# Kernel optimization log

Hardware: AMD Instinct MI355X
Metric: run time of the kernel (lower is better)

The kernel has to match this reference:

```python
import jax, jax.numpy as jnp
import numpy as np

EPS = 1e-5
DN = ('NCHW', 'OIHW', 'NCHW')

def _conv(x, w, b):
    y = jax.lax.conv_general_dilated(x, w, (1, 1), 'SAME', dimension_numbers=DN)
    return y + b.reshape(1, -1, 1, 1)

def _bn(x, g, bt, m, v):
    # inference-mode BatchNorm2d
    scale = g * jax.lax.rsqrt(v + EPS)
    return (x - m.reshape(1, -1, 1, 1)) * scale.reshape(1, -1, 1, 1) + bt.reshape(1, -1, 1, 1)


def setup_inputs() -> dict:
    key = jax.random.key(0)
    ks = jax.random.split(key, 12)
    B, C, H, W = 32, 1, 1024, 1024
    inp = {
        'x':  jax.random.normal(ks[0], (B, C, H, W), jnp.float32),
        # conv3x3_bn_r (shared module, used 3 times)
        'wa': jax.random.normal(ks[1], (1, 1, 3, 3), jnp.float32) * 0.2,
        'ba': jnp.zeros((1,), jnp.float32),
        'ga': jnp.ones((1,), jnp.float32),
        'bta': jnp.zeros((1,), jnp.float32),
        'ma': jax.random.normal(ks[2], (1,), jnp.float32) * 0.1,
        'va': jax.random.uniform(ks[3], (1,), jnp.float32) + 0.5,
        # conv3x3_bn
        'wb': jax.random.normal(ks[4], (1, 1, 3, 3), jnp.float32) * 0.2,
        'bb': jnp.zeros((1,), jnp.float32),
        'gb': jnp.ones((1,), jnp.float32),
        'btb': jnp.zeros((1,), jnp.float32),
        'mb': jax.random.normal(ks[5], (1,), jnp.float32) * 0.1,
        'vb': jax.random.uniform(ks[6], (1,), jnp.float32) + 0.5,
        # conv1x1_bn
        'wc': jax.random.normal(ks[7], (1, 1, 1, 1), jnp.float32) * 0.2,
        'bc': jnp.zeros((1,), jnp.float32),
        'gc': jnp.ones((1,), jnp.float32),
        'btc': jnp.zeros((1,), jnp.float32),
        'mc': jax.random.normal(ks[8], (1,), jnp.float32) * 0.1,
        'vc': jax.random.uniform(ks[9], (1,), jnp.float32) + 0.5,
        # conv3x3_r
        'wd': jax.random.normal(ks[10], (1, 1, 3, 3), jnp.float32) * 0.2,
        'bd': jnp.zeros((1,), jnp.float32),
        # conv1x1
        'we': jax.random.normal(ks[11], (1, 1, 1, 1), jnp.float32) * 0.2,
        'be': jnp.zeros((1,), jnp.float32),
    }
    return inp


def reference(x, wa, ba, ga, bta, ma, va, wb, bb, gb, btb, mb, vb,
              wc, bc, gc, btc, mc, vc, wd, bd, we, be):
    # t = 0 (top-left corner): right->left cummax + bottom->up cummax
    # conv3x3_bn_r is one shared module; x1 == x2 in the original.
    x1 = jax.nn.relu(_bn(_conv(x, wa, ba), ga, bta, ma, va))
    i1 = jax.lax.cummax(x1, axis=3, reverse=True)  # RightLeftMaxPooling
    i2 = jax.lax.cummax(x1, axis=2, reverse=True)  # DownUpMaxPooling
    b1 = _bn(_conv(i1 + i2, wb, bb), gb, btb, mb, vb)
    b2 = _bn(_conv(x, wc, bc), gc, btc, mc, vc)
    s = jax.nn.relu(b1 + b2)
    out = jax.nn.relu(_bn(_conv(s, wa, ba), ga, bta, ma, va))  # shared conv3x3_bn_r again
    out = jax.nn.relu(_conv(out, wd, bd))
    out = _conv(out, we, be)
    return out
```

## Files before the change

kernel.cpp:

```cpp
#include <hip/hip_runtime.h>
#include <math.h>

#define EPS 1e-5f
constexpr int IMG_H = 1024;
constexpr int IMG_W = 1024;
constexpr int NIMG  = 32;

__device__ __forceinline__ float frelu(float v) { return fmaxf(v, 0.f); }

__global__ __launch_bounds__(256) void k_front(
    const float* __restrict__ x,
    const float* __restrict__ wa, const float* __restrict__ ba,
    const float* __restrict__ ga, const float* __restrict__ bta,
    const float* __restrict__ ma, const float* __restrict__ va,
    float* __restrict__ M8, float* __restrict__ M8part, float* __restrict__ I1S)
{
    const int bid   = blockIdx.x;
    const int img   = bid >> 7;
    const int strip = bid & 127;
    const int lane  = threadIdx.x & 63;
    const int wv    = threadIdx.x >> 6;
    const int rb    = strip * 8 + wv * 2;

    const float scale = ga[0] * rsqrtf(va[0] + EPS);
    float w_s[9];
#pragma unroll
    for (int k = 0; k < 9; ++k) w_s[k] = wa[k] * scale;
    const float bias = (ba[0] - ma[0]) * scale + bta[0];

    const float* xim = x + (size_t)img * IMG_H * IMG_W;

    float4 X[4][4];
#pragma unroll
    for (int ri = 0; ri < 4; ++ri) {
        const int gr = rb - 1 + ri;
        if (gr >= 0 && gr < IMG_H) {
            const float4* rp = (const float4*)(xim + (size_t)gr * IMG_W);
#pragma unroll
            for (int q = 0; q < 4; ++q) X[ri][q] = rp[lane + 64 * q];
        } else {
#pragma unroll
            for (int q = 0; q < 4; ++q) X[ri][q] = make_float4(0.f, 0.f, 0.f, 0.f);
        }
    }

    float4 wm[4], w1r1[4];
#pragma unroll
    for (int rr = 0; rr < 2; ++rr) {
        float4 v[4];
#pragma unroll
        for (int q = 0; q < 4; ++q) {
            float acc0 = bias, acc1 = bias, acc2 = bias, acc3 = bias;
#pragma unroll
            for (int dy = 0; dy < 3; ++dy) {
                float4 C = X[rr + dy][q];
                float Lw = __shfl_up(C.w, 1, 64);
                float Bq = 0.f;
                if (q > 0) Bq = __shfl(X[rr + dy][q - 1].w, 63, 64);
                if (lane == 0) Lw = Bq;
                float Rx = __shfl_down(C.x, 1, 64);
                float Aq = 0.f;
                if (q < 3) Aq = __shfl(X[rr + dy][q + 1].x, 0, 64);
                if (lane == 63) Rx = Aq;
                const float w0 = w_s[3 * dy], w1 = w_s[3 * dy + 1], w2 = w_s[3 * dy + 2];
                acc0 += w0 * Lw  + w1 * C.x + w2 * C.y;
                acc1 += w0 * C.x + w1 * C.y + w2 * C.z;
                acc2 += w0 * C.y + w1 * C.z + w2 * C.w;
                acc3 += w0 * C.z + w1 * C.w + w2 * Rx;
            }
            v[q] = make_float4(frelu(acc0), frelu(acc1), frelu(acc2), frelu(acc3));
        }

        float sW[4], T4[4], e[4];
#pragma unroll
        for (int q = 0; q < 4; ++q) {
            float s3 = v[q].w;
            float s2 = fmaxf(v[q].z, s3);
            float s1 = fmaxf(v[q].y, s2);
            float s0 = fmaxf(v[q].x, s1);
            sW[q] = s3;
            float mm = s0;
#pragma unroll
            for (int off = 1; off < 64; off <<= 1) {
                float o = __shfl_down(mm, off, 64);
                if (lane + off < 64) mm = fmaxf(mm, o);
            }
            T4[q] = __shfl(mm, 0, 64);
            float ex = __shfl_down(mm, 1, 64);
            if (lane == 63) ex = -INFINITY;
            e[q] = ex;
        }
        float Rr[4];
        Rr[3] = -INFINITY;
        Rr[2] = T4[3];
        Rr[1] = fmaxf(T4[2], Rr[2]);
        Rr[0] = fmaxf(T4[1], Rr[1]);

        if ((lane & 7) == 0) {
            const int r = rb + rr;
#pragma unroll
            for (int q = 0; q < 4; ++q) {
                const float val = fmaxf(sW[q], fmaxf(e[q], Rr[q]));
                I1S[((size_t)img * IMG_H + r) * 32 + (q * 8 + (lane >> 3))] = val;
            }
        }

        if (rr == 0) {
#pragma unroll
            for (int q = 0; q < 4; ++q) wm[q] = v[q];
        } else {
#pragma unroll
            for (int q = 0; q < 4; ++q) {
                wm[q].x = fmaxf(wm[q].x, v[q].x); wm[q].y = fmaxf(wm[q].y, v[q].y);
                wm[q].z = fmaxf(wm[q].z, v[q].z); wm[q].w = fmaxf(wm[q].w, v[q].w);
            }
#pragma unroll
            for (int q = 0; q < 4; ++q) w1r1[q] = v[q];
        }
    }

    __shared__ float4 wmax[5][256];
#pragma unroll
    for (int q = 0; q < 4; ++q) wmax[wv][64 * q + lane] = wm[q];
    if (wv == 1) {
#pragma unroll
        for (int q = 0; q < 4; ++q) wmax[4][64 * q + lane] = w1r1[q];
    }
    __syncthreads();

    const int tid = threadIdx.x;
    float4 a0 = wmax[0][tid], a1 = wmax[1][tid], a2 = wmax[2][tid], a3 = wmax[3][tid];
    float4 f;
    f.x = fmaxf(fmaxf(a0.x, a1.x), fmaxf(a2.x, a3.x));
    f.y = fmaxf(fmaxf(a0.y, a1.y), fmaxf(a2.y, a3.y));
    f.z = fmaxf(fmaxf(a0.z, a1.z), fmaxf(a2.z, a3.z));
    f.w = fmaxf(fmaxf(a0.w, a1.w), fmaxf(a2.w, a3.w));
    ((float4*)(M8 + ((size_t)img * 128 + strip) * IMG_W))[tid] = f;

    if (strip >= 8 && (strip & 7) == 0) {
        float4 r3v = wmax[4][tid];
        float4 fp;
        fp.x = fmaxf(r3v.x, fmaxf(a2.x, a3.x));
        fp.y = fmaxf(r3v.y, fmaxf(a2.y, a3.y));
        fp.z = fmaxf(r3v.z, fmaxf(a2.z, a3.z));
        fp.w = fmaxf(r3v.w, fmaxf(a2.w, a3.w));
        ((float4*)(M8part + ((size_t)img * 15 + ((strip >> 3) - 1)) * IMG_W))[tid] = fp;
    }
}

__global__ __launch_bounds__(256) void k_seed2(
    const float* __restrict__ M8, const float* __restrict__ M8part,
    float* __restrict__ I2S)
{
    const int gid = blockIdx.x * 256 + threadIdx.x;
    const int img = gid >> 10;
    const int c   = gid & 1023;
    const float* mp = M8 + (size_t)img * 128 * IMG_W + c;

    float run = 0.f;
#pragma unroll 7
    for (int s = 127; s >= 9; --s) {
        run = fmaxf(run, mp[(size_t)s * IMG_W]);
        if ((s & 7) == 1) {
            const int m = (s - 9) >> 3;
            const size_t o = ((size_t)img * 15 + m) * IMG_W + c;
            I2S[o] = fmaxf(run, M8part[o]);
        }
    }
}

#define PITCH 44
__global__ __launch_bounds__(256, 6) void k_tile(
    const float* __restrict__ x,
    const float* __restrict__ I1S, const float* __restrict__ I2S,
    const float* __restrict__ wa, const float* __restrict__ ba,
    const float* __restrict__ ga, const float* __restrict__ bta,
    const float* __restrict__ ma, const float* __restrict__ va,
    const float* __restrict__ wb, const float* __restrict__ bb,
    const float* __restrict__ gb, const float* __restrict__ btb,
    const float* __restrict__ mb, const float* __restrict__ vb,
    const float* __restrict__ wc, const float* __restrict__ bc,
    const float* __restrict__ gcp, const float* __restrict__ btc,
    const float* __restrict__ mc, const float* __restrict__ vc,
    const float* __restrict__ wd, const float* __restrict__ bd,
    const float* __restrict__ we, const float* __restrict__ be,
    float* __restrict__ out)
{
    __shared__ float B1[70 * PITCH];
    __shared__ float B2[68 * PITCH];
    __shared__ float P[4][PITCH];

    const int bid = blockIdx.x;
    const int img = bid >> 9;
    const int tr  = (bid >> 5) & 15;
    const int tc  = bid & 31;
    const int r0  = tr * 64, c0 = tc * 32;
    const int tid = threadIdx.x;
    const int lane = tid & 63;
    const int wv   = tid >> 6;

    const float* xim = x + (size_t)img * IMG_H * IMG_W;

    float i2sv = 0.f;
    if (tr < 15 && lane < 38) {
        const int col = c0 - 3 + lane;
        if ((unsigned)col < (unsigned)IMG_W)
            i2sv = I2S[((size_t)img * 15 + tr) * IMG_W + col];
    }
    const int g0 = wv * 18;
    const int nrows = (wv == 3) ? 16 : 18;
    float seed1v = 0.f;
    if (lane < nrows && tc < 31) {
        const int row = r0 - 3 + g0 + lane;
        if ((unsigned)row < (unsigned)IMG_H)
            seed1v = I1S[((size_t)img * IMG_H + row) * 32 + (tc + 1)];
    }

    const float sa = ga[0] * rsqrtf(va[0] + EPS);
    float was[9];
#pragma unroll
    for (int k = 0; k < 9; ++k) was[k] = wa[k] * sa;
    const float biasa = (ba[0] - ma[0]) * sa + bta[0];

    const float sb = gb[0] * rsqrtf(vb[0] + EPS);
    float wbs[9];
#pragma unroll
    for (int k = 0; k < 9; ++k) wbs[k] = wb[k] * sb;
    const float biasb = (bb[0] - mb[0]) * sb + btb[0];

    const float sc = gcp[0] * rsqrtf(vc[0] + EPS);
    const float kc = wc[0] * sc;
    const float biasc = (bc[0] - mc[0]) * sc + btc[0];

    float wd9[9];
#pragma unroll
    for (int k = 0; k < 9; ++k) wd9[k] = wd[k];
    const float bd0 = bd[0], we0 = we[0], be0 = be[0];

    if (tid < 180) {
        const int mi = tid / 10, mj = tid - mi * 10;
        const int wr0 = mi * 4, wc0 = mj * 4;
        const int gr0 = r0 - 4 + wr0;
        const int gc0 = c0 - 4 + wc0;
        const bool fastC = (gc0 >= 0) && (gc0 + 5 < IMG_W);
        float w[6][6];
#pragma unroll
        for (int rr = 0; rr < 6; ++rr) {
            const int gr = gr0 + rr;
            if ((unsigned)gr < (unsigned)IMG_H) {
                const float* rp = xim + (size_t)gr * IMG_W;
                if (fastC) {
                    float4 a4 = *(const float4*)(rp + gc0);
                    float2 b2 = *(const float2*)(rp + gc0 + 4);
                    w[rr][0] = a4.x; w[rr][1] = a4.y; w[rr][2] = a4.z;
                    w[rr][3] = a4.w; w[rr][4] = b2.x; w[rr][5] = b2.y;
                } else {
#pragma unroll
                    for (int j = 0; j < 6; ++j) {
                        const int gc = gc0 + j;
                        w[rr][j] = ((unsigned)gc < (unsigned)IMG_W) ? rp[gc] : 0.f;
                    }
                }
            } else {
#pragma unroll
                for (int j = 0; j < 6; ++j) w[rr][j] = 0.f;
            }
        }
#pragma unroll
        for (int rr = 0; rr < 4; ++rr) {
            if (wr0 + rr < 70) {
                const int grx = r0 - 3 + wr0 + rr;
                float res4[4];
#pragma unroll
                for (int cc = 0; cc < 4; ++cc) {
                    float acc = biasa;
#pragma unroll
                    for (int dy = 0; dy < 3; ++dy)
#pragma unroll
                        for (int dx = 0; dx < 3; ++dx)
                            acc += was[3 * dy + dx] * w[rr + dy][cc + dx];
                    const int gcx = c0 - 3 + wc0 + cc;
                    float val = 0.f;
                    if ((unsigned)grx < (unsigned)IMG_H && (unsigned)gcx < (unsigned)IMG_W)
                        val = frelu(acc);
                    res4[cc] = val;
                }
                *(float4*)&B1[(wr0 + rr) * PITCH + wc0] =
                    make_float4(res4[0], res4[1], res4[2], res4[3]);
            }
        }
    }
    __syncthreads();

    {
        float pm = 0.f;
        if (lane < 38) {
            for (int k = 0; k < nrows; ++k)
                pm = fmaxf(pm, B1[(g0 + k) * PITCH + lane]);
            P[wv][lane] = pm;
        }
    }
    __syncthreads();

    {
        float run = i2sv;
#pragma unroll
        for (int w2 = 1; w2 < 4; ++w2)
            if (w2 > wv && lane < 38) run = fmaxf(run, P[w2][lane]);
#pragma unroll 6
        for (int k = 0; k < 18; ++k) {
            if (k < nrows) {
                const int lr = nrows - 1 - k;
                const int wr = g0 + lr;
                const float xv = (lane < 38) ? B1[wr * PITCH + lane] : 0.f;
                float mm = xv;
#pragma unroll
                for (int off = 1; off < 64; off <<= 1) {
                    float o = __shfl_down(mm, off, 64);
                    if (lane + off < 64) mm = fmaxf(mm, o);
                }
                const float sd = __shfl(seed1v, lr, 64);
                const float i1v = fmaxf(mm, sd);
                run = fmaxf(run, xv);
                const int row = r0 - 3 + wr;
                const int col = c0 - 3 + lane;
                const bool inb = ((unsigned)row < (unsigned)IMG_H) &&
                                 ((unsigned)col < (unsigned)IMG_W);
                if (lane < 38)
                    B1[wr * PITCH + lane] = inb ? (i1v + run) : 0.f;
            }
        }
    }
    __syncthreads();

    if (tid < 153) {
        const int mi = tid / 9, mj = tid - mi * 9;
        const int si0 = mi * 4, sj0 = mj * 4;
        float win[6][6];
#pragma unroll
        for (int r = 0; r < 6; ++r) {
            const float* p = &B1[(si0 + r) * PITCH + sj0];
            float4 a4 = *(const float4*)p;
            float2 b2 = *(const float2*)(p + 4);
            win[r][0] = a4.x; win[r][1] = a4.y; win[r][2] = a4.z;
            win[r][3] = a4.w; win[r][4] = b2.x; win[r][5] = b2.y;
        }
#pragma unroll
        for (int a = 0; a < 4; ++a) {
            float res4[4];
#pragma unroll
            for (int b = 0; b < 4; ++b) {
                float acc = biasb;
#pragma unroll
                for (int dy = 0; dy < 3; ++dy)
#pragma unroll
                    for (int dx = 0; dx < 3; ++dx)
                        acc += wbs[3 * dy + dx] * win[a + dy][b + dx];
                const int gr = r0 - 2 + si0 + a, gc = c0 - 2 + sj0 + b;
                float sres = 0.f;
                if ((unsigned)gr < (unsigned)IMG_H && (unsigned)gc < (unsigned)IMG_W) {
                    const float xv = xim[(size_t)gr * IMG_W + gc];
                    sres = frelu(acc + xv * kc + biasc);
                }
                res4[b] = sres;
            }
            *(float4*)&B2[(si0 + a) * PITCH + sj0] =
                make_float4(res4[0], res4[1], res4[2], res4[3]);
        }
    }
    __syncthreads();

    if (tid < 153) {
        const int mi = tid / 9, mj = tid - mi * 9;
        const int ai0 = mi * 4, aj0 = mj * 4;
        float win[6][6];
#pragma unroll
        for (int r = 0; r < 6; ++r) {
            const int rrow = (ai0 + r < 68) ? (ai0 + r) : 67;
            const float* p = &B2[rrow * PITCH + aj0];
            float4 a4 = *(const float4*)p;
            float2 b2 = *(const float2*)(p + 4);
            win[r][0] = a4.x; win[r][1] = a4.y; win[r][2] = a4.z;
            win[r][3] = a4.w; win[r][4] = b2.x; win[r][5] = b2.y;
        }
#pragma unroll
        for (int a = 0; a < 4; ++a) {
            if (ai0 + a < 66) {
                float res4[4];
#pragma unroll
                for (int b = 0; b < 4; ++b) {
                    float acc = biasa;
#pragma unroll
                    for (int dy = 0; dy < 3; ++dy)
#pragma unroll
                        for (int dx = 0; dx < 3; ++dx)
                            acc += was[3 * dy + dx] * win[a + dy][b + dx];
                    const int gr = r0 - 1 + ai0 + a, gc = c0 - 1 + aj0 + b;
                    float r1 = 0.f;
                    if ((unsigned)gr < (unsigned)IMG_H && (unsigned)gc < (unsigned)IMG_W)
                        r1 = frelu(acc);
                    res4[b] = r1;
                }
                *(float4*)&B1[(ai0 + a) * PITCH + aj0] =
                    make_float4(res4[0], res4[1], res4[2], res4[3]);
            }
        }
    }
    __syncthreads();

    {
        const int oi0 = (tid >> 3) * 2, oj0 = (tid & 7) * 4;
        float win[4][6];
#pragma unroll
        for (int r = 0; r < 4; ++r) {
            const float* p = &B1[(oi0 + r) * PITCH + oj0];
            float4 a4 = *(const float4*)p;
            float2 b2 = *(const float2*)(p + 4);
            win[r][0] = a4.x; win[r][1] = a4.y; win[r][2] = a4.z;
            win[r][3] = a4.w; win[r][4] = b2.x; win[r][5] = b2.y;
        }
        float* oim = out + (size_t)img * IMG_H * IMG_W;
#pragma unroll
        for (int a = 0; a < 2; ++a) {
            float res4[4];
#pragma unroll
            for (int b = 0; b < 4; ++b) {
                float acc = bd0;
#pragma unroll
                for (int dy = 0; dy < 3; ++dy)
#pragma unroll
                    for (int dx = 0; dx < 3; ++dx)
                        acc += wd9[3 * dy + dx] * win[a + dy][b + dx];
                res4[b] = frelu(acc) * we0 + be0;
            }
            *(float4*)&oim[(size_t)(r0 + oi0 + a) * IMG_W + (c0 + oj0)] =
                make_float4(res4[0], res4[1], res4[2], res4[3]);
        }
    }
}

extern "C" void kernel_launch(void* const* d_in, const int* in_sizes, int n_in,
                              void* d_out, int out_size, void* d_ws, size_t ws_size,
                              hipStream_t stream)
{
    const float* x   = (const float*)d_in[0];
    const float* wa  = (const float*)d_in[1];
    const float* ba  = (const float*)d_in[2];
    const float* ga  = (const float*)d_in[3];
    const float* bta = (const float*)d_in[4];
    const float* ma  = (const float*)d_in[5];
    const float* va  = (const float*)d_in[6];
    const float* wb  = (const float*)d_in[7];
    const float* bb  = (const float*)d_in[8];
    const float* gb  = (const float*)d_in[9];
    const float* btb = (const float*)d_in[10];
    const float* mb  = (const float*)d_in[11];
    const float* vb  = (const float*)d_in[12];
    const float* wc  = (const float*)d_in[13];
    const float* bc  = (const float*)d_in[14];
    const float* gcp = (const float*)d_in[15];
    const float* btc = (const float*)d_in[16];
    const float* mc  = (const float*)d_in[17];
    const float* vc  = (const float*)d_in[18];
    const float* wd  = (const float*)d_in[19];
    const float* bd  = (const float*)d_in[20];
    const float* we  = (const float*)d_in[21];
    const float* be  = (const float*)d_in[22];

    float* outp   = (float*)d_out;
    float* M8     = (float*)d_ws;
    float* M8part = M8 + (size_t)NIMG * 128 * IMG_W;
    float* I1S    = M8part + (size_t)NIMG * 15 * IMG_W;
    float* I2S    = I1S + (size_t)NIMG * IMG_H * 32;

    k_front<<<dim3(NIMG * 128), dim3(256), 0, stream>>>(
        x, wa, ba, ga, bta, ma, va, M8, M8part, I1S);
    k_seed2<<<dim3(128), dim3(256), 0, stream>>>(M8, M8part, I2S);
    k_tile<<<dim3(NIMG * 16 * 32), dim3(256), 0, stream>>>(
        x, I1S, I2S, wa, ba, ga, bta, ma, va, wb, bb, gb, btb, mb, vb,
        wc, bc, gcp, btc, mc, vc, wd, bd, we, be, outp);
}
```

Baseline: 511.9 us.

## Stage input tile in shared memory and reuse it for the 1x1 branch

Loads the 72x40 input halo tile into a new shared buffer BA with coalesced float4 loads, replacing the per-thread overlapping global 6x6 window loads. The conv1x1 branch then reads x from this shared tile into registers instead of issuing scalar global loads. After that, BA is reused as the storage that B2 used to have, which keeps total LDS about the same. Interior tiles skip the per-pixel image-boundary checks. The cost is an extra barrier and a 16-float register array that could add register pressure at 6 blocks per CU.

```diff
diff --git a/kernel.cpp b/kernel.cpp
--- a/kernel.cpp
+++ b/kernel.cpp
@@ -186,9 +186,9 @@
     const float* __restrict__ we, const float* __restrict__ be,
     float* __restrict__ out)
 {
+    __shared__ float BA[72 * PITCH];
     __shared__ float B1[70 * PITCH];
-    __shared__ float B2[68 * PITCH];
-    __shared__ float P[4][PITCH];
+    __shared__ float Pm[4][PITCH];
 
     const int bid = blockIdx.x;
     const int img = bid >> 9;
@@ -198,6 +198,7 @@
     const int tid = threadIdx.x;
     const int lane = tid & 63;
     const int wv   = tid >> 6;
+    const bool intr = (tr >= 1) && (tr <= 14) && (tc >= 1) && (tc <= 30);
 
     const float* xim = x + (size_t)img * IMG_H * IMG_W;
 
@@ -237,39 +238,59 @@
     for (int k = 0; k < 9; ++k) wd9[k] = wd[k];
     const float bd0 = bd[0], we0 = we[0], be0 = be[0];
 
+    if (intr) {
+        const float* xs = xim + (size_t)(r0 - 4) * IMG_W + (c0 - 4);
+#pragma unroll
+        for (int it = 0; it < 3; ++it) {
+            const int f = tid + it * 256;
+            if (f < 720) {
+                const int row = f / 10, cg = f - row * 10;
+                float4 v = *(const float4*)(xs + (size_t)row * IMG_W + 4 * cg);
+                *(float4*)&BA[row * PITCH + 4 * cg] = v;
+            }
+        }
+    } else {
+#pragma unroll
+        for (int it = 0; it < 3; ++it) {
+            const int f = tid + it * 256;
+            if (f < 720) {
+                const int row = f / 10, cg = f - row * 10;
+                const int gr = r0 - 4 + row;
+                const int gc = c0 - 4 + 4 * cg;
+                float4 v = make_float4(0.f, 0.f, 0.f, 0.f);
+                if ((unsigned)gr < (unsigned)IMG_H) {
+                    const float* rp = xim + (size_t)gr * IMG_W;
+                    if (gc >= 0 && gc + 3 < IMG_W) {
+                        v = *(const float4*)(rp + gc);
+                    } else {
+                        if ((unsigned)(gc)     < (unsigned)IMG_W) v.x = rp[gc];
+                        if ((unsigned)(gc + 1) < (unsigned)IMG_W) v.y = rp[gc + 1];
+                        if ((unsigned)(gc + 2) < (unsigned)IMG_W) v.z = rp[gc + 2];
+                        if ((unsigned)(gc + 3) < (unsigned)IMG_W) v.w = rp[gc + 3];
+                    }
+                }
+                *(float4*)&BA[row * PITCH + 4 * cg] = v;
+            }
+        }
+    }
+    __syncthreads();
+
     if (tid < 180) {
         const int mi = tid / 10, mj = tid - mi * 10;
         const int wr0 = mi * 4, wc0 = mj * 4;
-        const int gr0 = r0 - 4 + wr0;
-        const int gc0 = c0 - 4 + wc0;
-        const bool fastC = (gc0 >= 0) && (gc0 + 5 < IMG_W);
         float w[6][6];
 #pragma unroll
-        for (int rr = 0; rr < 6; ++rr) {
-            const int gr = gr0 + rr;
-            if ((unsigned)gr < (unsigned)IMG_H) {
-                const float* rp = xim + (size_t)gr * IMG_W;
-                if (fastC) {
-                    float4 a4 = *(const float4*)(rp + gc0);
-                    float2 b2 = *(const float2*)(rp + gc0 + 4);
-                    w[rr][0] = a4.x; w[rr][1] = a4.y; w[rr][2] = a4.z;
-                    w[rr][3] = a4.w; w[rr][4] = b2.x; w[rr][5] = b2.y;
-                } else {
-#pragma unroll
-                    for (int j = 0; j < 6; ++j) {
-                        const int gc = gc0 + j;
-                        w[rr][j] = ((unsigned)gc < (unsigned)IMG_W) ? rp[gc] : 0.f;
-                    }
-                }
-            } else {
-#pragma unroll
-                for (int j = 0; j < 6; ++j) w[rr][j] = 0.f;
-            }
+        for (int r = 0; r < 6; ++r) {
+            const int br = (wr0 + r < 72) ? (wr0 + r) : 71;
+            const float* p = &BA[br * PITCH + wc0];
+            float4 a4 = *(const float4*)p;
+            float2 b2 = *(const float2*)(p + 4);
+            w[r][0] = a4.x; w[r][1] = a4.y; w[r][2] = a4.z;
+            w[r][3] = a4.w; w[r][4] = b2.x; w[r][5] = b2.y;
         }
 #pragma unroll
         for (int rr = 0; rr < 4; ++rr) {
             if (wr0 + rr < 70) {
-                const int grx = r0 - 3 + wr0 + rr;
                 float res4[4];
 #pragma unroll
                 for (int cc = 0; cc < 4; ++cc) {
@@ -279,11 +300,16 @@
 #pragma unroll
                         for (int dx = 0; dx < 3; ++dx)
                             acc += was[3 * dy + dx] * w[rr + dy][cc + dx];
-                    const int gcx = c0 - 3 + wc0 + cc;
-                    float val = 0.f;
-                    if ((unsigned)grx < (unsigned)IMG_H && (unsigned)gcx < (unsigned)IMG_W)
-                        val = frelu(acc);
-                    res4[cc] = val;
+                    if (intr) {
+                        res4[cc] = frelu(acc);
+                    } else {
+                        const int grx = r0 - 3 + wr0 + rr;
+                        const int gcx = c0 - 3 + wc0 + cc;
+                        float val = 0.f;
+                        if ((unsigned)grx < (unsigned)IMG_H && (unsigned)gcx < (unsigned)IMG_W)
+                            val = frelu(acc);
+                        res4[cc] = val;
+                    }
                 }
                 *(float4*)&B1[(wr0 + rr) * PITCH + wc0] =
                     make_float4(res4[0], res4[1], res4[2], res4[3]);
@@ -297,7 +323,7 @@
         if (lane < 38) {
             for (int k = 0; k < nrows; ++k)
                 pm = fmaxf(pm, B1[(g0 + k) * PITCH + lane]);
-            P[wv][lane] = pm;
+            Pm[wv][lane] = pm;
         }
     }
     __syncthreads();
@@ -306,7 +332,7 @@
         float run = i2sv;
 #pragma unroll
         for (int w2 = 1; w2 < 4; ++w2)
-            if (w2 > wv && lane < 38) run = fmaxf(run, P[w2][lane]);
+            if (w2 > wv && lane < 38) run = fmaxf(run, Pm[w2][lane]);
 #pragma unroll 6
         for (int k = 0; k < 18; ++k) {
             if (k < nrows) {
@@ -333,38 +359,56 @@
     }
     __syncthreads();
 
+    float xr[16];
     if (tid < 153) {
         const int mi = tid / 9, mj = tid - mi * 9;
         const int si0 = mi * 4, sj0 = mj * 4;
-        float win[6][6];
+#pragma unroll
+        for (int a = 0; a < 4; ++a) {
+            const float* p = &BA[(si0 + 2 + a) * PITCH + sj0 + 2];
+            float2 u = *(const float2*)p;
+            float2 v = *(const float2*)(p + 2);
+            xr[a * 4 + 0] = u.x; xr[a * 4 + 1] = u.y;
+            xr[a * 4 + 2] = v.x; xr[a * 4 + 3] = v.y;
+        }
+    }
+    __syncthreads();
+
+    if (tid < 153) {
+        const int mi = tid / 9, mj = tid - mi * 9;
+        const int si0 = mi * 4, sj0 = mj * 4;
+        float w[6][6];
 #pragma unroll
         for (int r = 0; r < 6; ++r) {
             const float* p = &B1[(si0 + r) * PITCH + sj0];
             float4 a4 = *(const float4*)p;
             float2 b2 = *(const float2*)(p + 4);
-            win[r][0] = a4.x; win[r][1] = a4.y; win[r][2] = a4.z;
-            win[r][3] = a4.w; win[r][4] = b2.x; win[r][5] = b2.y;
+            w[r][0] = a4.x; w[r][1] = a4.y; w[r][2] = a4.z;
+            w[r][3] = a4.w; w[r][4] = b2.x; w[r][5] = b2.y;
         }
 #pragma unroll
         for (int a = 0; a < 4; ++a) {
             float res4[4];
 #pragma unroll
             for (int b = 0; b < 4; ++b) {
-                float acc = biasb;
+                float acc = biasb + biasc;
 #pragma unroll
                 for (int dy = 0; dy < 3; ++dy)
 #pragma unroll
                     for (int dx = 0; dx < 3; ++dx)
-                        acc += wbs[3 * dy + dx] * win[a + dy][b + dx];
-                const int gr = r0 - 2 + si0 + a, gc = c0 - 2 + sj0 + b;
-                float sres = 0.f;
-                if ((unsigned)gr < (unsigned)IMG_H && (unsigned)gc < (unsigned)IMG_W) {
-                    const float xv = xim[(size_t)gr * IMG_W + gc];
-                    sres = frelu(acc + xv * kc + biasc);
+                        acc += wbs[3 * dy + dx] * w[a + dy][b + dx];
+                acc += xr[a * 4 + b] * kc;
+                if (intr) {
+                    res4[b] = frelu(acc);
+                } else {
+                    const int gr = r0 - 2 + si0 + a, gc = c0 - 2 + sj0 + b;
+                    float sres = 0.f;
+                    if ((unsigned)gr < (unsigned)IMG_H && (unsigned)gc < (unsigned)IMG_W)
+                        sres = frelu(acc);
+                    res4[b] = sres;
                 }
-                res4[b] = sres;
-            }
-            *(float4*)&B2[(si0 + a) * PITCH + sj0] =
+            }
+            *(float4*)&BA[(si0 + a) * PITCH + sj0] =
                 make_float4(res4[0], res4[1], res4[2], res4[3]);
         }
     }
@@ -373,15 +417,15 @@
     if (tid < 153) {
         const int mi = tid / 9, mj = tid - mi * 9;
         const int ai0 = mi * 4, aj0 = mj * 4;
-        float win[6][6];
+        float w[6][6];
 #pragma unroll
         for (int r = 0; r < 6; ++r) {
             const int rrow = (ai0 + r < 68) ? (ai0 + r) : 67;
-            const float* p = &B2[rrow * PITCH + aj0];
+            const float* p = &BA[rrow * PITCH + aj0];
             float4 a4 = *(const float4*)p;
             float2 b2 = *(const float2*)(p + 4);
-            win[r][0] = a4.x; win[r][1] = a4.y; win[r][2] = a4.z;
-            win[r][3] = a4.w; win[r][4] = b2.x; win[r][5] = b2.y;
+            w[r][0] = a4.x; w[r][1] = a4.y; w[r][2] = a4.z;
+            w[r][3] = a4.w; w[r][4] = b2.x; w[r][5] = b2.y;
         }
 #pragma unroll
         for (int a = 0; a < 4; ++a) {
@@ -394,12 +438,16 @@
                     for (int dy = 0; dy < 3; ++dy)
 #pragma unroll
                         for (int dx = 0; dx < 3; ++dx)
-                            acc += was[3 * dy + dx] * win[a + dy][b + dx];
-                    const int gr = r0 - 1 + ai0 + a, gc = c0 - 1 + aj0 + b;
-                    float r1 = 0.f;
-                    if ((unsigned)gr < (unsigned)IMG_H && (unsigned)gc < (unsigned)IMG_W)
-                        r1 = frelu(acc);
-                    res4[b] = r1;
+                            acc += was[3 * dy + dx] * w[a + dy][b + dx];
+                    if (intr) {
+                        res4[b] = frelu(acc);
+                    } else {
+                        const int gr = r0 - 1 + ai0 + a, gc = c0 - 1 + aj0 + b;
+                        float r1 = 0.f;
+                        if ((unsigned)gr < (unsigned)IMG_H && (unsigned)gc < (unsigned)IMG_W)
+                            r1 = frelu(acc);
+                        res4[b] = r1;
+                    }
                 }
                 *(float4*)&B1[(ai0 + a) * PITCH + aj0] =
                     make_float4(res4[0], res4[1], res4[2], res4[3]);
@@ -410,14 +458,14 @@
 
     {
         const int oi0 = (tid >> 3) * 2, oj0 = (tid & 7) * 4;
-        float win[4][6];
+        float w[4][6];
 #pragma unroll
         for (int r = 0; r < 4; ++r) {
             const float* p = &B1[(oi0 + r) * PITCH + oj0];
             float4 a4 = *(const float4*)p;
             float2 b2 = *(const float2*)(p + 4);
-            win[r][0] = a4.x; win[r][1] = a4.y; win[r][2] = a4.z;
-            win[r][3] = a4.w; win[r][4] = b2.x; win[r][5] = b2.y;
+            w[r][0] = a4.x; w[r][1] = a4.y; w[r][2] = a4.z;
+            w[r][3] = a4.w; w[r][4] = b2.x; w[r][5] = b2.y;
         }
         float* oim = out + (size_t)img * IMG_H * IMG_W;
 #pragma unroll
@@ -430,7 +478,7 @@
                 for (int dy = 0; dy < 3; ++dy)
 #pragma unroll
                     for (int dx = 0; dx < 3; ++dx)
-                        acc += wd9[3 * dy + dx] * win[a + dy][b + dx];
+                        acc += wd9[3 * dy + dx] * w[a + dy][b + dx];
                 res4[b] = frelu(acc) * we0 + be0;
             }
             *(float4*)&oim[(size_t)(r0 + oi0 + a) * IMG_W + (c0 + oj0)] =
```

Result: faster. 494.0 us (-3.5%).
